# Kernel tuning notes

Hardware: AMD Instinct MI355X
Metric: run time of the kernel (lower is better)

The kernel has to match this reference:

```python
import jax, jax.numpy as jnp
import numpy as np

N = 50000
E = 800000
IN_DIM = 128
HID = 128
HEADS = 8
OUT_DIM = 64
NEG_SLOPE = 0.2


def setup_inputs() -> dict:
    key = jax.random.key(0)
    ks = jax.random.split(key, 12)
    x = jax.random.normal(ks[0], (N, IN_DIM), dtype=jnp.float32)
    edge_index = jax.random.randint(ks[1], (2, E), 0, N, dtype=jnp.int64)
    C1 = HID // HEADS  # per-head out dim of layer 1
    s1 = 1.0 / np.sqrt(IN_DIM)
    s2 = 1.0 / np.sqrt(HID)
    W1 = jax.random.uniform(ks[2], (IN_DIM, HEADS * C1), jnp.float32, -s1, s1)
    a_src1 = jax.random.uniform(ks[3], (HEADS, C1), jnp.float32, -1.0, 1.0)
    a_dst1 = jax.random.uniform(ks[4], (HEADS, C1), jnp.float32, -1.0, 1.0)
    b1 = jnp.zeros((HEADS * C1,), jnp.float32)
    W2 = jax.random.uniform(ks[5], (HID, OUT_DIM), jnp.float32, -s2, s2)
    a_src2 = jax.random.uniform(ks[6], (1, OUT_DIM), jnp.float32, -1.0, 1.0)
    a_dst2 = jax.random.uniform(ks[7], (1, OUT_DIM), jnp.float32, -1.0, 1.0)
    b2 = jnp.zeros((OUT_DIM,), jnp.float32)
    return {"x": x, "edge_index": edge_index, "W1": W1, "a_src1": a_src1,
            "a_dst1": a_dst1, "b1": b1, "W2": W2, "a_src2": a_src2,
            "a_dst2": a_dst2, "b2": b2}


def gat_conv(x, src, dst, W, a_s, a_d, b, n_heads, c_head):
    # Linear projection per head: [N, H, C]
    h = (x @ W).reshape(N, n_heads, c_head)
    # Per-node attention terms: [N, H]
    alpha_s = jnp.einsum('nhc,hc->nh', h, a_s)
    alpha_d = jnp.einsum('nhc,hc->nh', h, a_d)
    # Per-edge raw scores: [Etot, H]
    score = jax.nn.leaky_relu(alpha_s[src] + alpha_d[dst], negative_slope=NEG_SLOPE)
    # Segment softmax over edges sharing the same destination
    m = jax.ops.segment_max(score, dst, num_segments=N)
    e = jnp.exp(score - m[dst])
    denom = jax.ops.segment_sum(e, dst, num_segments=N)
    alpha = e / denom[dst]  # every node has a self-loop -> denom > 0
    # Weighted aggregation: scatter-add alpha * h_src into destinations
    out = jax.ops.segment_sum(alpha[:, :, None] * h[src], dst, num_segments=N)
    return out.reshape(N, n_heads * c_head) + b


def reference(x, edge_index, W1, a_src1, a_dst1, b1, W2, a_src2, a_dst2, b2):
    # add self loops (GATConv add_self_loops=True)
    loops = jnp.arange(N, dtype=edge_index.dtype)
    src = jnp.concatenate([edge_index[0], loops])
    dst = jnp.concatenate([edge_index[1], loops])
    C1 = HID // HEADS
    h = gat_conv(x, src, dst, W1, a_src1, a_dst1, b1, HEADS, C1)
    h = jax.nn.elu(h)  # dropout = 0 (eval)
    out = gat_conv(h, src, dst, W2, a_src2, a_dst2, b2, 1, OUT_DIM)
    return jax.nn.log_softmax(out, axis=-1)
```

## Files before the change

kernel.cpp:

```cpp
#include <hip/hip_runtime.h>
#include <math.h>

typedef unsigned int  u32;
typedef unsigned short u16;
typedef short bf16x8 __attribute__((ext_vector_type(8)));
typedef float f32x4  __attribute__((ext_vector_type(4)));

#define NN    50000
#define NE    800000
#define ET    (NE + NN)
#define IND   128
#define HIDD  128
#define NH    8
#define OD    64
#define SLOPE 0.2f

#define NB    196
#define EPB   4096
#define NBB   ((NE + EPB - 1) / EPB)
#define LCAP  64
#define CAPB  5120
#define CPAD  16
#define BSTRIDE 7168

#define W1EXT 144
#define W2EXT 80

__device__ __forceinline__ u32 bf16rne(float f) {
    u32 u = __float_as_uint(f);
    return (u + 0x7fffu + ((u >> 16) & 1u)) >> 16;
}

#define LR(s) fmaxf((s), SLOPE * (s))

__global__ __launch_bounds__(256) void k_bin(
    const int* __restrict__ ei, int* __restrict__ cnt, u32* __restrict__ staging)
{
    __shared__ u32 lbuf[NB * LCAP];
    __shared__ int lcnt[NB];
    __shared__ int gbase[NB];
    const int t = threadIdx.x;
    const int e0 = blockIdx.x * EPB;

    for (int i = t; i < NB; i += 256) lcnt[i] = 0;
    __syncthreads();

    for (int i = t; i < EPB; i += 256) {
        const int e = e0 + i;
        if (e >= NE) break;
        const int src = ei[e];
        const int dst = ei[NE + e];
        const int b = dst >> 8;
        const int p = atomicAdd(&lcnt[b], 1);
        lbuf[b * LCAP + p] = ((u32)(dst & 255) << 16) | (u32)src;
    }
    __syncthreads();

    for (int i = t; i < NB; i += 256)
        gbase[i] = atomicAdd(&cnt[i * CPAD], lcnt[i]);
    __syncthreads();

    for (int b = t; b < NB; b += 256) {
        const int n = lcnt[b];
        const int gb = gbase[b];
        u32* dstp = staging + (size_t)b * CAPB + gb;
        const u32* srcp = lbuf + b * LCAP;
        for (int j = 0; j < n; ++j) dstp[j] = srcp[j];
    }
}

__global__ __launch_bounds__(1024) void k_place(
    const int* __restrict__ cnt, const u32* __restrict__ staging,
    int* __restrict__ rowptr, int* __restrict__ rowend,
    u16* __restrict__ sorted16)
{
    __shared__ int hist[256];
    __shared__ int cur[256];
    __shared__ int scan[256];
    const int b = blockIdx.x;
    const int t = threadIdx.x;
    const int tot = cnt[b * CPAD];
    const int base = b * BSTRIDE;

    if (t < 256) hist[t] = ((b * 256 + t) < NN) ? 1 : 0;
    __syncthreads();

    for (int i = t; i < tot; i += 1024)
        atomicAdd(&hist[staging[(size_t)b * CAPB + i] >> 16], 1);
    __syncthreads();

    if (t < 256) scan[t] = (hist[t] + 7) & ~7;
    __syncthreads();
    for (int off = 1; off < 256; off <<= 1) {
        int v = 0;
        if (t < 256 && t >= off) v = scan[t - off];
        __syncthreads();
        if (t < 256) scan[t] += v;
        __syncthreads();
    }
    if (t < 256) {
        const int padded = (hist[t] + 7) & ~7;
        const int excl = (t == 0) ? 0 : scan[t - 1];
        const int node = b * 256 + t;
        if (node < NN) {
            rowptr[node] = base + excl;
            rowend[node] = base + excl + padded;
            sorted16[base + excl] = (u16)node;
            for (int j = hist[t]; j < padded; ++j)
                sorted16[base + excl + j] = (u16)NN;
            cur[t] = excl + 1;
        } else {
            cur[t] = excl;
        }
    }
    __syncthreads();
    for (int i = t; i < tot; i += 1024) {
        const u32 v = staging[(size_t)b * CAPB + i];
        const int pos = atomicAdd(&cur[v >> 16], 1);
        sorted16[base + pos] = (u16)(v & 0xffffu);
    }
}

__global__ __launch_bounds__(256) void k_wprep(
    const float* __restrict__ W1, const float* __restrict__ W2,
    const float* __restrict__ as1w, const float* __restrict__ ad1w,
    const float* __restrict__ as2w, const float* __restrict__ ad2w,
    u16* __restrict__ Wt1, u16* __restrict__ Wt2, int* __restrict__ cnt,
    u32* __restrict__ h1b, float* __restrict__ as1, float* __restrict__ as2)
{
    const int i = blockIdx.x * 256 + threadIdx.x;
    if (i < NB * CPAD) cnt[i] = 0;
    if (i < 64) h1b[(size_t)64 * NN + i] = 0;
    if (i < 8)  as1[(size_t)NH * NN + i] = -1e30f;
    if (i == 8) as2[NN] = -1e30f;

    if (i < W1EXT * 128) {
        const int j = i >> 7, k = i & 127;
        float v;
        if (j < 128) {
            v = W1[k * 128 + j];
        } else if (j < 136) {
            const int h = j - 128;
            v = 0.f;
            for (int c = 0; c < 16; ++c)
                v += W1[k * 128 + h * 16 + c] * as1w[h * 16 + c];
        } else {
            const int h = j - 136;
            v = 0.f;
            for (int c = 0; c < 16; ++c)
                v += W1[k * 128 + h * 16 + c] * ad1w[h * 16 + c];
        }
        Wt1[j * 128 + k] = (u16)bf16rne(v);
    } else if (i < W1EXT * 128 + W2EXT * 128) {
        const int i2 = i - W1EXT * 128;
        const int j = i2 >> 7, k = i2 & 127;
        float v = 0.f;
        if (j < 64) {
            v = W2[k * 64 + j];
        } else if (j == 64) {
            for (int c = 0; c < 64; ++c) v += W2[k * 64 + c] * as2w[c];
        } else if (j == 65) {
            for (int c = 0; c < 64; ++c) v += W2[k * 64 + c] * ad2w[c];
        }
        Wt2[j * 128 + k] = (u16)bf16rne(v);
    }
}

__global__ __launch_bounds__(512) void k_gemm1(
    const float* __restrict__ x, const u16* __restrict__ Wt1,
    u16* __restrict__ h1s, float* __restrict__ as1, float* __restrict__ ad1)
{
    __shared__ u32 xb[128 * 64];
    __shared__ u32 Wb[W1EXT * 64];
    const int tid = threadIdx.x;
    const int row0 = blockIdx.x * 128;

    {
        const uint4* Wt = (const uint4*)Wt1;
        for (int p = 0; p < 5; ++p) {
            const int id = p * 512 + tid;
            if (id < W1EXT * 16) {
                const int n = id >> 4, c = id & 15;
                *(uint4*)(Wb + n * 64 + ((c ^ (n & 15)) << 2)) = Wt[n * 16 + c];
            }
        }
    }
    for (int p = 0; p < 4; ++p) {
        const int id = p * 512 + tid;
        const int m = id >> 4, c = id & 15;
        const int row = row0 + m;
        uint4 v = make_uint4(0, 0, 0, 0);
        if (row < NN) {
            const float4 f0 = *(const float4*)(x + (size_t)row * 128 + c * 8);
            const float4 f1 = *(const float4*)(x + (size_t)row * 128 + c * 8 + 4);
            v.x = bf16rne(f0.x) | (bf16rne(f0.y) << 16);
            v.y = bf16rne(f0.z) | (bf16rne(f0.w) << 16);
            v.z = bf16rne(f1.x) | (bf16rne(f1.y) << 16);
            v.w = bf16rne(f1.z) | (bf16rne(f1.w) << 16);
        }
        *(uint4*)(xb + m * 64 + ((c ^ (m & 15)) << 2)) = v;
    }
    __syncthreads();

    const int w = tid >> 6, lane = tid & 63;
    const int nl = lane & 15, quad = lane >> 4;
    f32x4 acc[9] = {};
    for (int kk = 0; kk < 4; ++kk) {
        const int cm = kk * 4 + quad;
        const bf16x8 a = *(const bf16x8*)(xb + (16 * w + nl) * 64 + ((cm ^ nl) << 2));
#pragma unroll
        for (int tn = 0; tn < 9; ++tn) {
            const bf16x8 b = *(const bf16x8*)(Wb + (16 * tn + nl) * 64 + ((cm ^ nl) << 2));
            acc[tn] = __builtin_amdgcn_mfma_f32_16x16x32_bf16(a, b, acc[tn], 0, 0, 0);
        }
    }

#pragma unroll
    for (int tn = 0; tn < 8; ++tn) {
#pragma unroll
        for (int r = 0; r < 4; ++r) {
            const int row = row0 + 16 * w + quad * 4 + r;
            if (row < NN)
                h1s[(size_t)row * 128 + 16 * tn + nl] = (u16)bf16rne(acc[tn][r]);
        }
    }
#pragma unroll
    for (int r = 0; r < 4; ++r) {
        const int row = row0 + 16 * w + quad * 4 + r;
        if (row < NN) {
            const float v = acc[8][r];
            if (nl < 8) as1[row * NH + nl] = v;
            else        ad1[row * NH + (nl - 8)] = v;
        }
    }
}

__global__ __launch_bounds__(512) void k_gemm2(
    const u32* __restrict__ act2b, const u16* __restrict__ Wt2,
    u16* __restrict__ h2s, float* __restrict__ as2, float* __restrict__ ad2)
{
    __shared__ u32 xb[128 * 64];
    __shared__ u32 Wb[W2EXT * 64];
    const int tid = threadIdx.x;
    const int row0 = blockIdx.x * 128;

    {
        const uint4* Wt = (const uint4*)Wt2;
        for (int p = 0; p < 3; ++p) {
            const int id = p * 512 + tid;
            if (id < W2EXT * 16) {
                const int n = id >> 4, c = id & 15;
                *(uint4*)(Wb + n * 64 + ((c ^ (n & 15)) << 2)) = Wt[n * 16 + c];
            }
        }
    }
    for (int p = 0; p < 4; ++p) {
        const int id = p * 512 + tid;
        const int m = id >> 4, c = id & 15;
        const int row = row0 + m;
        uint4 v = make_uint4(0, 0, 0, 0);
        if (row < NN) v = ((const uint4*)act2b)[(size_t)row * 16 + c];
        *(uint4*)(xb + m * 64 + ((c ^ (m & 15)) << 2)) = v;
    }
    __syncthreads();

    const int w = tid >> 6, lane = tid & 63;
    const int nl = lane & 15, quad = lane >> 4;
    f32x4 acc[5] = {};
    for (int kk = 0; kk < 4; ++kk) {
        const int cm = kk * 4 + quad;
        const bf16x8 a = *(const bf16x8*)(xb + (16 * w + nl) * 64 + ((cm ^ nl) << 2));
#pragma unroll
        for (int tn = 0; tn < 5; ++tn) {
            const bf16x8 b = *(const bf16x8*)(Wb + (16 * tn + nl) * 64 + ((cm ^ nl) << 2));
            acc[tn] = __builtin_amdgcn_mfma_f32_16x16x32_bf16(a, b, acc[tn], 0, 0, 0);
        }
    }

#pragma unroll
    for (int tn = 0; tn < 4; ++tn) {
#pragma unroll
        for (int r = 0; r < 4; ++r) {
            const int row = row0 + 16 * w + quad * 4 + r;
            if (row < NN)
                h2s[(size_t)row * 64 + 16 * tn + nl] = (u16)bf16rne(acc[tn][r]);
        }
    }
#pragma unroll
    for (int r = 0; r < 4; ++r) {
        const int row = row0 + 16 * w + quad * 4 + r;
        if (row < NN) {
            const float v = acc[4][r];
            if (nl == 0) as2[row] = v;
            else if (nl == 1) ad2[row] = v;
        }
    }
}

#define PG1(KK, S, G, WJ) do {                                                \
    const uint4 p = *(const uint4*)(sorted16 + (KK));                         \
    S[0] = p.x & 0xffffu; S[1] = p.x >> 16;                                   \
    S[2] = p.y & 0xffffu; S[3] = p.y >> 16;                                   \
    S[4] = p.z & 0xffffu; S[5] = p.z >> 16;                                   \
    S[6] = p.w & 0xffffu; S[7] = p.w >> 16;                                   \
    const u32 hlf = (head & 4) ? ((head & 2) ? p.w : p.z)                     \
                               : ((head & 2) ? p.y : p.x);                    \
    const u32 sj = (head & 1) ? (hlf >> 16) : (hlf & 0xffffu);                \
    WJ = __expf(LR(as1[sj * NH + eh] + adeh));                                \
    _Pragma("unroll") for (int j = 0; j < 8; ++j)                             \
        G[j] = h1b[S[j] * 64 + lane];                                         \
} while (0)

#define CONS1(G, WJ) do {                                                     \
    _Pragma("unroll") for (int j = 0; j < 8; ++j) {                           \
        const float wv = __uint_as_float((u32)__builtin_amdgcn_ds_bpermute(   \
            h4 + j * 32, (int)__float_as_uint(WJ)));                          \
        acc0 += wv * __uint_as_float(G[j] << 16);                             \
        acc1 += wv * __uint_as_float(G[j] & 0xffff0000u);                     \
        den  += wv; }                                                         \
} while (0)

__global__ __launch_bounds__(256) void k_agg1(
    const int* __restrict__ rowptr, const int* __restrict__ rowend,
    const u16* __restrict__ sorted16,
    const u32* __restrict__ h1b, const float* __restrict__ as1,
    const float* __restrict__ ad1,
    u32* __restrict__ act2b)
{
    const int node = blockIdx.x * 4 + (threadIdx.x >> 6);
    const int lane = threadIdx.x & 63;
    const int head = lane >> 3;
    const int eh   = lane & 7;
    const float adeh = ad1[node * NH + eh];
    const int k0 = rowptr[node], kend = rowend[node];
    const int h4 = head << 2;
    float acc0 = 0.f, acc1 = 0.f, den = 0.f;
    u32 sA[8], gA[8], sB[8], gB[8];
    float wA, wB;

    PG1(k0, sA, gA, wA);
    int k = k0 + 8;
    while (k + 16 <= kend) {
        PG1(k, sB, gB, wB);      CONS1(gA, wA);
        PG1(k + 8, sA, gA, wA);  CONS1(gB, wB);
        k += 16;
    }
    if (k < kend) {
        PG1(k, sB, gB, wB);  CONS1(gA, wA);  CONS1(gB, wB);
    } else {
        CONS1(gA, wA);
    }

    const float inv = 1.f / den;
    float v0 = acc0 * inv, v1 = acc1 * inv;
    v0 = v0 > 0.f ? v0 : expm1f(v0);
    v1 = v1 > 0.f ? v1 : expm1f(v1);
    act2b[node * 64 + lane] = bf16rne(v0) | (bf16rne(v1) << 16);
}

#define PG2(KK, S, G, WJ) do {                                                \
    const uint4 p = *(const uint4*)(sorted16 + (KK));                         \
    S[0] = p.x & 0xffffu; S[1] = p.x >> 16;                                   \
    S[2] = p.y & 0xffffu; S[3] = p.y >> 16;                                   \
    S[4] = p.z & 0xffffu; S[5] = p.z >> 16;                                   \
    S[6] = p.w & 0xffffu; S[7] = p.w >> 16;                                   \
    const u32 hlf = (lane & 4) ? ((lane & 2) ? p.w : p.z)                     \
                               : ((lane & 2) ? p.y : p.x);                    \
    const u32 sj = (lane & 1) ? (hlf >> 16) : (hlf & 0xffffu);                \
    WJ = __expf(LR(as2[sj] + adv));                                           \
    _Pragma("unroll") for (int j = 0; j < 8; ++j)                             \
        G[j] = h2s[S[j] * 64 + lane];                                         \
} while (0)

#define CONS2(G, WJ) do {                                                     \
    _Pragma("unroll") for (int j = 0; j < 8; ++j) {                           \
        const float wv = __uint_as_float((u32)__builtin_amdgcn_ds_bpermute(   \
            j << 2, (int)__float_as_uint(WJ)));                               \
        acc += wv * __uint_as_float(((u32)G[j]) << 16);                       \
        den += wv; }                                                          \
} while (0)

__global__ __launch_bounds__(256) void k_agg2(
    const int* __restrict__ rowptr, const int* __restrict__ rowend,
    const u16* __restrict__ sorted16,
    const u16* __restrict__ h2s, const float* __restrict__ as2,
    const float* __restrict__ ad2,
    float* __restrict__ out)
{
    const int node = blockIdx.x * 4 + (threadIdx.x >> 6);
    const int lane = threadIdx.x & 63;
    const float adv = ad2[node];
    const int k0 = rowptr[node], kend = rowend[node];
    float acc = 0.f, den = 0.f;
    u32 sA[8], gA[8], sB[8], gB[8];
    float wA, wB;

    PG2(k0, sA, gA, wA);
    int k = k0 + 8;
    while (k + 16 <= kend) {
        PG2(k, sB, gB, wB);      CONS2(gA, wA);
        PG2(k + 8, sA, gA, wA);  CONS2(gB, wB);
        k += 16;
    }
    if (k < kend) {
        PG2(k, sB, gB, wB);  CONS2(gA, wA);  CONS2(gB, wB);
    } else {
        CONS2(gA, wA);
    }

    const float v = acc / den;
    float m = v;
    for (int kk = 1; kk < 64; kk <<= 1) m = fmaxf(m, __shfl_xor(m, kk));
    float se = __expf(v - m);
    for (int kk = 1; kk < 64; kk <<= 1) se += __shfl_xor(se, kk);
    out[node * 64 + lane] = v - m - logf(se);
}

extern "C" void kernel_launch(void* const* d_in, const int* in_sizes, int n_in,
                              void* d_out, int out_size, void* d_ws, size_t ws_size,
                              hipStream_t stream)
{
    (void)in_sizes; (void)n_in; (void)out_size; (void)ws_size;
    const float* x    = (const float*)d_in[0];
    const int*   ei   = (const int*)d_in[1];
    const float* W1   = (const float*)d_in[2];
    const float* as1w = (const float*)d_in[3];
    const float* ad1w = (const float*)d_in[4];
    const float* W2   = (const float*)d_in[6];
    const float* as2w = (const float*)d_in[7];
    const float* ad2w = (const float*)d_in[8];
    float* out = (float*)d_out;

    u32* ws = (u32*)d_ws;
    size_t o = 0;
    auto take = [&](size_t n) { size_t r = o; o += (n + 15) & ~(size_t)15; return r; };

    u32*   h1b      = ws + take((size_t)64 * (NN + 1));
    float* as1      = (float*)(ws + take((size_t)NH * NN + 8));
    float* ad1      = (float*)(ws + take((size_t)NH * NN));
    u32*   act2b    = ws + take((size_t)64 * NN);
    float* as2      = (float*)(ws + take(NN + 1));
    float* ad2      = (float*)(ws + take(NN));
    int*   rowptr   = (int*)(ws + take(NN));
    int*   rowend   = (int*)(ws + take(NN));
    u16*   sorted16 = (u16*)(ws + take(((size_t)NB * BSTRIDE + 1) / 2));
    u32*   staging  = ws + take((size_t)NB * CAPB);
    int*   cnt      = (int*)(ws + take(NB * CPAD));
    u16*   Wt1      = (u16*)(ws + take((size_t)W1EXT * 128 / 2));
    u16*   Wt2      = (u16*)(ws + take((size_t)W2EXT * 128 / 2));
    u16*   h1s      = (u16*)h1b;
    u16*   h2s      = (u16*)h1b;

    k_wprep<<<112, 256, 0, stream>>>(W1, W2, as1w, ad1w, as2w, ad2w,
                                     Wt1, Wt2, cnt, h1b, as1, as2);
    k_bin  <<<NBB, 256, 0, stream>>>(ei, cnt, staging);
    k_place<<<NB, 1024, 0, stream>>>(cnt, staging, rowptr, rowend, sorted16);

    k_gemm1<<<391, 512, 0, stream>>>(x, Wt1, h1s, as1, ad1);
    k_agg1 <<<NN / 4, 256, 0, stream>>>(rowptr, rowend, sorted16, h1b, as1, ad1, act2b);
    k_gemm2<<<391, 512, 0, stream>>>(act2b, Wt2, h2s, as2, ad2);
    k_agg2 <<<NN / 4, 256, 0, stream>>>(rowptr, rowend, sorted16, h2s, as2, ad2, out);
}
```

Baseline: 191.2 us.

## Fuse independent prep kernels and stage GEMM outputs through LDS for coalesced stores

Weight preparation now runs as extra blocks of the edge-binning kernel, and CSR placement runs as extra blocks of the first GEMM, so independent work shares a launch and the kernel count drops. The counter zeroing moves to a hipMemsetAsync. Both GEMM kernels now write their bf16 outputs into shared memory first and then copy them out as row-contiguous 16-byte stores, replacing scattered 2-byte global writes. The placement blocks run with 512 instead of 1024 threads, and the extra block syncs in the GEMMs add a little latency.

```diff
diff --git a/kernel.cpp b/kernel.cpp
--- a/kernel.cpp
+++ b/kernel.cpp
@@ -25,6 +25,8 @@
 
 #define W1EXT 144
 #define W2EXT 80
+#define WPB   112
+#define G1B   391
 
 __device__ __forceinline__ u32 bf16rne(float f) {
     u32 u = __float_as_uint(f);
@@ -33,15 +35,59 @@
 
 #define LR(s) fmaxf((s), SLOPE * (s))
 
-__global__ __launch_bounds__(256) void k_bin(
-    const int* __restrict__ ei, int* __restrict__ cnt, u32* __restrict__ staging)
+__global__ __launch_bounds__(256) void k_prep_bin(
+    const int* __restrict__ ei, int* __restrict__ cnt, u32* __restrict__ staging,
+    const float* __restrict__ W1, const float* __restrict__ W2,
+    const float* __restrict__ as1w, const float* __restrict__ ad1w,
+    const float* __restrict__ as2w, const float* __restrict__ ad2w,
+    u16* __restrict__ Wt1, u16* __restrict__ Wt2,
+    u32* __restrict__ h1b, float* __restrict__ as1, float* __restrict__ as2)
 {
     __shared__ u32 lbuf[NB * LCAP];
     __shared__ int lcnt[NB];
     __shared__ int gbase[NB];
     const int t = threadIdx.x;
+
+    if (blockIdx.x >= NBB) {
+        const int i = (blockIdx.x - NBB) * 256 + t;
+        if (i < 64) h1b[(size_t)64 * NN + i] = 0;
+        if (i < 8)  as1[(size_t)NH * NN + i] = -1e30f;
+        if (i == 8) as2[NN] = -1e30f;
+
+        if (i < W1EXT * 128) {
+            const int j = i >> 7, k = i & 127;
+            float v;
+            if (j < 128) {
+                v = W1[k * 128 + j];
+            } else if (j < 136) {
+                const int h = j - 128;
+                v = 0.f;
+                for (int c = 0; c < 16; ++c)
+                    v += W1[k * 128 + h * 16 + c] * as1w[h * 16 + c];
+            } else {
+                const int h = j - 136;
+                v = 0.f;
+                for (int c = 0; c < 16; ++c)
+                    v += W1[k * 128 + h * 16 + c] * ad1w[h * 16 + c];
+            }
+            Wt1[j * 128 + k] = (u16)bf16rne(v);
+        } else if (i < W1EXT * 128 + W2EXT * 128) {
+            const int i2 = i - W1EXT * 128;
+            const int j = i2 >> 7, k = i2 & 127;
+            float v = 0.f;
+            if (j < 64) {
+                v = W2[k * 64 + j];
+            } else if (j == 64) {
+                for (int c = 0; c < 64; ++c) v += W2[k * 64 + c] * as2w[c];
+            } else if (j == 65) {
+                for (int c = 0; c < 64; ++c) v += W2[k * 64 + c] * ad2w[c];
+            }
+            Wt2[j * 128 + k] = (u16)bf16rne(v);
+        }
+        return;
+    }
+
     const int e0 = blockIdx.x * EPB;
-
     for (int i = t; i < NB; i += 256) lcnt[i] = 0;
     __syncthreads();
 
@@ -69,111 +115,66 @@
     }
 }
 
-__global__ __launch_bounds__(1024) void k_place(
+__global__ __launch_bounds__(512) void k_place_gemm1(
     const int* __restrict__ cnt, const u32* __restrict__ staging,
     int* __restrict__ rowptr, int* __restrict__ rowend,
-    u16* __restrict__ sorted16)
-{
-    __shared__ int hist[256];
-    __shared__ int cur[256];
-    __shared__ int scan[256];
-    const int b = blockIdx.x;
-    const int t = threadIdx.x;
-    const int tot = cnt[b * CPAD];
-    const int base = b * BSTRIDE;
-
-    if (t < 256) hist[t] = ((b * 256 + t) < NN) ? 1 : 0;
-    __syncthreads();
-
-    for (int i = t; i < tot; i += 1024)
-        atomicAdd(&hist[staging[(size_t)b * CAPB + i] >> 16], 1);
-    __syncthreads();
-
-    if (t < 256) scan[t] = (hist[t] + 7) & ~7;
-    __syncthreads();
-    for (int off = 1; off < 256; off <<= 1) {
-        int v = 0;
-        if (t < 256 && t >= off) v = scan[t - off];
-        __syncthreads();
-        if (t < 256) scan[t] += v;
-        __syncthreads();
-    }
-    if (t < 256) {
-        const int padded = (hist[t] + 7) & ~7;
-        const int excl = (t == 0) ? 0 : scan[t - 1];
-        const int node = b * 256 + t;
-        if (node < NN) {
-            rowptr[node] = base + excl;
-            rowend[node] = base + excl + padded;
-            sorted16[base + excl] = (u16)node;
-            for (int j = hist[t]; j < padded; ++j)
-                sorted16[base + excl + j] = (u16)NN;
-            cur[t] = excl + 1;
-        } else {
-            cur[t] = excl;
-        }
-    }
-    __syncthreads();
-    for (int i = t; i < tot; i += 1024) {
-        const u32 v = staging[(size_t)b * CAPB + i];
-        const int pos = atomicAdd(&cur[v >> 16], 1);
-        sorted16[base + pos] = (u16)(v & 0xffffu);
-    }
-}
-
-__global__ __launch_bounds__(256) void k_wprep(
-    const float* __restrict__ W1, const float* __restrict__ W2,
-    const float* __restrict__ as1w, const float* __restrict__ ad1w,
-    const float* __restrict__ as2w, const float* __restrict__ ad2w,
-    u16* __restrict__ Wt1, u16* __restrict__ Wt2, int* __restrict__ cnt,
-    u32* __restrict__ h1b, float* __restrict__ as1, float* __restrict__ as2)
-{
-    const int i = blockIdx.x * 256 + threadIdx.x;
-    if (i < NB * CPAD) cnt[i] = 0;
-    if (i < 64) h1b[(size_t)64 * NN + i] = 0;
-    if (i < 8)  as1[(size_t)NH * NN + i] = -1e30f;
-    if (i == 8) as2[NN] = -1e30f;
-
-    if (i < W1EXT * 128) {
-        const int j = i >> 7, k = i & 127;
-        float v;
-        if (j < 128) {
-            v = W1[k * 128 + j];
-        } else if (j < 136) {
-            const int h = j - 128;
-            v = 0.f;
-            for (int c = 0; c < 16; ++c)
-                v += W1[k * 128 + h * 16 + c] * as1w[h * 16 + c];
-        } else {
-            const int h = j - 136;
-            v = 0.f;
-            for (int c = 0; c < 16; ++c)
-                v += W1[k * 128 + h * 16 + c] * ad1w[h * 16 + c];
-        }
-        Wt1[j * 128 + k] = (u16)bf16rne(v);
-    } else if (i < W1EXT * 128 + W2EXT * 128) {
-        const int i2 = i - W1EXT * 128;
-        const int j = i2 >> 7, k = i2 & 127;
-        float v = 0.f;
-        if (j < 64) {
-            v = W2[k * 64 + j];
-        } else if (j == 64) {
-            for (int c = 0; c < 64; ++c) v += W2[k * 64 + c] * as2w[c];
-        } else if (j == 65) {
-            for (int c = 0; c < 64; ++c) v += W2[k * 64 + c] * ad2w[c];
-        }
-        Wt2[j * 128 + k] = (u16)bf16rne(v);
-    }
-}
-
-__global__ __launch_bounds__(512) void k_gemm1(
+    u16* __restrict__ sorted16,
     const float* __restrict__ x, const u16* __restrict__ Wt1,
     u16* __restrict__ h1s, float* __restrict__ as1, float* __restrict__ ad1)
 {
     __shared__ u32 xb[128 * 64];
     __shared__ u32 Wb[W1EXT * 64];
     const int tid = threadIdx.x;
-    const int row0 = blockIdx.x * 128;
+
+    if (blockIdx.x < NB) {
+        int* hist = (int*)xb;
+        int* cur  = hist + 256;
+        int* scan = cur + 256;
+        const int b = blockIdx.x;
+        const int tot = cnt[b * CPAD];
+        const int base = b * BSTRIDE;
+
+        if (tid < 256) hist[tid] = ((b * 256 + tid) < NN) ? 1 : 0;
+        __syncthreads();
+
+        for (int i = tid; i < tot; i += 512)
+            atomicAdd(&hist[staging[(size_t)b * CAPB + i] >> 16], 1);
+        __syncthreads();
+
+        if (tid < 256) scan[tid] = (hist[tid] + 7) & ~7;
+        __syncthreads();
+        for (int off = 1; off < 256; off <<= 1) {
+            int v = 0;
+            if (tid < 256 && tid >= off) v = scan[tid - off];
+            __syncthreads();
+            if (tid < 256) scan[tid] += v;
+            __syncthreads();
+        }
+        if (tid < 256) {
+            const int padded = (hist[tid] + 7) & ~7;
+            const int excl = (tid == 0) ? 0 : scan[tid - 1];
+            const int node = b * 256 + tid;
+            if (node < NN) {
+                rowptr[node] = base + excl;
+                rowend[node] = base + excl + padded;
+                sorted16[base + excl] = (u16)node;
+                for (int j = hist[tid]; j < padded; ++j)
+                    sorted16[base + excl + j] = (u16)NN;
+                cur[tid] = excl + 1;
+            } else {
+                cur[tid] = excl;
+            }
+        }
+        __syncthreads();
+        for (int i = tid; i < tot; i += 512) {
+            const u32 v = staging[(size_t)b * CAPB + i];
+            const int pos = atomicAdd(&cur[v >> 16], 1);
+            sorted16[base + pos] = (u16)(v & 0xffffu);
+        }
+        return;
+    }
+
+    const int row0 = (blockIdx.x - NB) * 128;
 
     {
         const uint4* Wt = (const uint4*)Wt1;
@@ -215,13 +216,16 @@
         }
     }
 
-#pragma unroll
-    for (int tn = 0; tn < 8; ++tn) {
-#pragma unroll
-        for (int r = 0; r < 4; ++r) {
-            const int row = row0 + 16 * w + quad * 4 + r;
-            if (row < NN)
-                h1s[(size_t)row * 128 + 16 * tn + nl] = (u16)bf16rne(acc[tn][r]);
+    __syncthreads();
+    {
+        u16* h1ld = (u16*)xb;
+#pragma unroll
+        for (int tn = 0; tn < 8; ++tn) {
+#pragma unroll
+            for (int r = 0; r < 4; ++r) {
+                const int row = 16 * w + quad * 4 + r;
+                h1ld[row * 128 + 16 * tn + nl] = (u16)bf16rne(acc[tn][r]);
+            }
         }
     }
 #pragma unroll
@@ -232,6 +236,14 @@
             if (nl < 8) as1[row * NH + nl] = v;
             else        ad1[row * NH + (nl - 8)] = v;
         }
+    }
+    __syncthreads();
+    for (int p = 0; p < 4; ++p) {
+        const int id = p * 512 + tid;
+        const int row = id >> 4, c = id & 15;
+        const int grow = row0 + row;
+        if (grow < NN)
+            ((uint4*)h1s)[(size_t)grow * 16 + c] = ((const uint4*)xb)[row * 16 + c];
     }
 }
 
@@ -277,13 +289,16 @@
         }
     }
 
-#pragma unroll
-    for (int tn = 0; tn < 4; ++tn) {
-#pragma unroll
-        for (int r = 0; r < 4; ++r) {
-            const int row = row0 + 16 * w + quad * 4 + r;
-            if (row < NN)
-                h2s[(size_t)row * 64 + 16 * tn + nl] = (u16)bf16rne(acc[tn][r]);
+    __syncthreads();
+    {
+        u16* h2ld = (u16*)xb;
+#pragma unroll
+        for (int tn = 0; tn < 4; ++tn) {
+#pragma unroll
+            for (int r = 0; r < 4; ++r) {
+                const int row = 16 * w + quad * 4 + r;
+                h2ld[row * 64 + 16 * tn + nl] = (u16)bf16rne(acc[tn][r]);
+            }
         }
     }
 #pragma unroll
@@ -294,6 +309,14 @@
             if (nl == 0) as2[row] = v;
             else if (nl == 1) ad2[row] = v;
         }
+    }
+    __syncthreads();
+    for (int p = 0; p < 2; ++p) {
+        const int id = p * 512 + tid;
+        const int row = id >> 3, c = id & 7;
+        const int grow = row0 + row;
+        if (grow < NN)
+            ((uint4*)h2s)[(size_t)grow * 8 + c] = ((const uint4*)xb)[row * 8 + c];
     }
 }
 
@@ -451,13 +474,16 @@
     u16*   h1s      = (u16*)h1b;
     u16*   h2s      = (u16*)h1b;
 
-    k_wprep<<<112, 256, 0, stream>>>(W1, W2, as1w, ad1w, as2w, ad2w,
-                                     Wt1, Wt2, cnt, h1b, as1, as2);
-    k_bin  <<<NBB, 256, 0, stream>>>(ei, cnt, staging);
-    k_place<<<NB, 1024, 0, stream>>>(cnt, staging, rowptr, rowend, sorted16);
-
-    k_gemm1<<<391, 512, 0, stream>>>(x, Wt1, h1s, as1, ad1);
-    k_agg1 <<<NN / 4, 256, 0, stream>>>(rowptr, rowend, sorted16, h1b, as1, ad1, act2b);
-    k_gemm2<<<391, 512, 0, stream>>>(act2b, Wt2, h2s, as2, ad2);
-    k_agg2 <<<NN / 4, 256, 0, stream>>>(rowptr, rowend, sorted16, h2s, as2, ad2, out);
-}
+    hipMemsetAsync(cnt, 0, NB * CPAD * sizeof(int), stream);
+
+    k_prep_bin<<<NBB + WPB, 256, 0, stream>>>(
+        ei, cnt, staging, W1, W2, as1w, ad1w, as2w, ad2w,
+        Wt1, Wt2, h1b, as1, as2);
+
+    k_place_gemm1<<<NB + G1B, 512, 0, stream>>>(
+        cnt, staging, rowptr, rowend, sorted16, x, Wt1, h1s, as1, ad1);
+
+    k_agg1<<<NN / 4, 256, 0, stream>>>(rowptr, rowend, sorted16, h1b, as1, ad1, act2b);
+    k_gemm2<<<G1B, 512, 0, stream>>>(act2b, Wt2, h2s, as2, ad2);
+    k_agg2<<<NN / 4, 256, 0, stream>>>(rowptr, rowend, sorted16, h2s, as2, ad2, out);
+}
```

Result: faster. 183.5 us (-4.0%).
